# Performance work log

Hardware: AMD Instinct MI355X
Metric: run time of the kernel (lower is better)

The kernel has to match this reference:

```python
import jax, jax.numpy as jnp
import numpy as np

# pywt db4 reconstruction low-pass (rec_lo) coefficients.
_H = np.array([
    0.23037781330885523, 0.7148465705525415, 0.6308807679295904,
    -0.02798376941698385, -0.18703481171888114, 0.030841381835986965,
    0.032883011666982945, -0.010597401784997278], dtype=np.float64)
# pywt dec_lo = _H[::-1]; conv (flipped) correlation kernel = dec_lo[::-1] = _H.
_FLO = _H
# dec_hi[k] = (-1)^(7-k) * _H[k]; correlation kernel = dec_hi[::-1] -> (-1)^k * _H[7-k].
_FHI = np.array([(-1.0) ** k * _H[7 - k] for k in range(8)])
_FILT = jnp.asarray(np.stack([_FLO, _FHI])[:, None, :], dtype=jnp.float32)  # [2,1,8]
_PAD = 7  # filter_len - 1
_LEVEL = 4


def _dwt_step(sig):
    """One pywt dwt level, mode='symmetric'. sig: [N, L] -> (cA, cD), each [N, (L+7)//2]."""
    # symmetric (half-sample) extension by filter_len-1 each side, drop first sample
    # so that stride-2 VALID correlation reproduces pywt's output phase/length.
    xp = jnp.pad(sig, ((0, 0), (_PAD, _PAD)), mode='symmetric')[:, 1:]
    out = jax.lax.conv_general_dilated(
        xp[:, None, :], _FILT, window_strides=(2,), padding='VALID',
        dimension_numbers=('NCH', 'OIH', 'NCH'))  # [N, 2, (L+7)//2]
    return out[:, 0, :], out[:, 1, :]


def setup_inputs() -> dict:
    key = jax.random.key(0)
    x = jax.random.normal(key, (64, 4096, 32), dtype=jnp.float32)  # [B, L, C]
    return {"x": x}


def reference(x):
    """Faithful batched version of pywt.wavedec(x[i,:,j], 'db4', 'symmetric', level=4).
    Returns tuple (cA4, cD4, cD3, cD2, cD1), each [B, C, scale_len]."""
    B, L, C = x.shape
    sig = jnp.transpose(x, (0, 2, 1)).reshape(B * C, L)
    details = []
    for _ in range(_LEVEL):
        sig, cd = _dwt_step(sig)
        details.append(cd)
    coeffs = [sig] + details[::-1]  # [cA_L, cD_L, ..., cD_1] like pywt.wavedec
    return tuple(c.reshape(B, C, c.shape[-1]) for c in coeffs)
```

## Files before the change

### kernel.cpp

```cpp
#include <hip/hip_runtime.h>


#define NT 256
#define NCHB 2

#define LPX 634
#define LP1 322
#define LP2 166
#define LP3 86
#define CDPA 314
#define CDPB 154
#define CAP4 40

#define L0C 4096
#define L1C 2051
#define L2C 1029
#define L3C 518
#define L4C 262
#define SC 2048

#define OFF_CD4 (SC * L4C)
#define OFF_CD3 (2 * SC * L4C)
#define OFF_CD2 (OFF_CD3 + SC * L3C)
#define OFF_CD1 (OFF_CD2 + SC * L2C)

__device__ __forceinline__ void filt8(
    const float w0, const float w1, const float w2, const float w3,
    const float w4, const float w5, const float w6, const float w7,
    float& a, float& d) {
    constexpr float FLO[8] = {
        0.23037781330885523f,  0.7148465705525415f,  0.6308807679295904f,
        -0.02798376941698385f, -0.18703481171888114f, 0.030841381835986965f,
        0.032883011666982945f, -0.010597401784997278f};
    constexpr float FHI[8] = {
        -0.010597401784997278f, -0.032883011666982945f, 0.030841381835986965f,
        0.18703481171888114f,  -0.02798376941698385f,  -0.6308807679295904f,
        0.7148465705525415f,   -0.23037781330885523f};
    float a0 = FLO[0] * w0;
    a0 = fmaf(FLO[1], w1, a0); a0 = fmaf(FLO[2], w2, a0); a0 = fmaf(FLO[3], w3, a0);
    float a1 = FLO[4] * w4;
    a1 = fmaf(FLO[5], w5, a1); a1 = fmaf(FLO[6], w6, a1); a1 = fmaf(FLO[7], w7, a1);
    a = a0 + a1;
    float d0 = FHI[0] * w0;
    d0 = fmaf(FHI[1], w1, d0); d0 = fmaf(FHI[2], w2, d0); d0 = fmaf(FHI[3], w3, d0);
    float d1 = FHI[4] * w4;
    d1 = fmaf(FHI[5], w5, d1); d1 = fmaf(FHI[6], w6, d1); d1 = fmaf(FHI[7], w7, d1);
    d = d0 + d1;
}

template <int R, bool LAST>
__device__ __forceinline__ void level_run(
    const float* __restrict__ src, int PS, int srclo,
    float* __restrict__ dst, int PD, int DL,
    int lo, int hi,
    float* __restrict__ cdbuf, int CDP,
    float* __restrict__ cabuf,
    int c, int slot) {
    const int span = hi - lo;
    int i0r = slot * R;
    if (i0r > span - R) i0r = span - R;
    const int i0 = lo + i0r;

    const float2* row2 = reinterpret_cast<const float2*>(src + c * PS);
    int p = i0 - (srclo >> 1);
    float2 f0 = row2[p], f1 = row2[p + 1], f2 = row2[p + 2];
    float* drow = LAST ? nullptr : dst + c * PD;
    float* cdrow = cdbuf + c * CDP - lo;
    float* carow = LAST ? cabuf + c * CAP4 - lo : nullptr;

#pragma unroll
    for (int r = 0; r < R; ++r) {
        const float2 f3 = row2[p + 3 + r];
        const int i = i0 + r;
        float a, d;
        filt8(f0.x, f0.y, f1.x, f1.y, f2.x, f2.y, f3.x, f3.y, a, d);

        if constexpr (!LAST) {
            drow[i - lo + 6] = a;
            if (lo == 0 && i < 6) drow[5 - i] = a;
            if (hi == DL && i >= DL - 7) drow[(2 * DL - 1 - i) - lo + 6] = a;
        } else {
            carow[i] = a;
        }
        cdrow[i] = d;
        f0 = f1; f1 = f2; f2 = f3;
    }
}

__device__ __forceinline__ void dump_rows(
    const float* __restrict__ buf, int pitch, int bufLo,
    float* __restrict__ gbase, int rowLen, int ownLo, int ownHi, int tid) {
    const int span = ownHi - ownLo;
#pragma unroll
    for (int c2 = 0; c2 < NCHB; ++c2) {
        float* g = gbase + (size_t)c2 * rowLen + ownLo;
        const float* s = buf + c2 * pitch + (ownLo - bufLo);
        for (int i = tid; i < span; i += NT) g[i] = s[i];
    }
}

__global__ __launch_bounds__(NT, 8) void fused_dwt_kernel(
    const float* __restrict__ x, float* __restrict__ out) {
    __shared__ __align__(16) float bx[NCHB * LPX];
    __shared__ __align__(16) float b1[NCHB * LP1];
    __shared__ __align__(16) float b2[NCHB * LP2];
    __shared__ __align__(16) float b3[NCHB * LP3];
    __shared__ __align__(16) float cdA[NCHB * CDPA];
    __shared__ __align__(16) float cdB[NCHB * CDPB];
    __shared__ __align__(16) float caB[NCHB * CAP4];

    const int bid = blockIdx.x;
    const int work = (bid & 7) * 1024 + (bid >> 3);
    const int cg = work & 15;
    const int tile = (work >> 4) & 7;
    const int b = work >> 7;

    const int tid = threadIdx.x;
    const int c = tid & 1;
    const int slot = tid >> 1;
    const int c0 = cg * 2;
    const int sigB = b * 32 + c0;

    const int lo4 = 33 * tile, hi4 = min(L4C, lo4 + 33);
    const int lo3 = max(0, 2 * lo4 - 6), hi3 = min(L3C, 2 * hi4);
    const int lo2 = max(0, 2 * lo3 - 6), hi2 = min(L2C, 2 * hi3);
    const int lo1 = max(0, 2 * lo2 - 6), hi1 = min(L1C, 2 * hi2);
    const int lox = max(0, 2 * lo1 - 6), hix = min(L0C, 2 * hi1);

    const float* xb = x + (size_t)b * (L0C * 32) + c0;
    const int npair = (hix - lox) >> 1;
    for (int q = tid; q < npair; q += NT) {
        const int j = q << 1;
        const int t = lox + j;
        const float2 va = *reinterpret_cast<const float2*>(xb + (size_t)t * 32);
        const float2 vb = *reinterpret_cast<const float2*>(xb + (size_t)(t + 1) * 32);
        const float avv[2] = {va.x, va.y};
        const float bvv[2] = {vb.x, vb.y};
#pragma unroll
        for (int hh = 0; hh < NCHB; ++hh)
            *reinterpret_cast<float2*>(bx + hh * LPX + 6 + j) = make_float2(avv[hh], bvv[hh]);
        if (lox == 0 && t < 6) {
#pragma unroll
            for (int hh = 0; hh < NCHB; ++hh) {
                bx[hh * LPX + 5 - t] = avv[hh];
                if (t + 1 < 6) bx[hh * LPX + 4 - t] = bvv[hh];
            }
        }
        if (hix == L0C && t + 1 >= L0C - 7) {
#pragma unroll
            for (int hh = 0; hh < NCHB; ++hh) {
                if (t >= L0C - 7) bx[hh * LPX + (2 * L0C - 1 - t) - lox + 6] = avv[hh];
                bx[hh * LPX + (2 * L0C - 2 - t) - lox + 6] = bvv[hh];
            }
        }
    }
    __syncthreads();

    float* gca4 = out + (size_t)sigB * L4C;
    float* gcd4 = out + OFF_CD4 + (size_t)sigB * L4C;
    float* gcd3 = out + OFF_CD3 + (size_t)sigB * L3C;
    float* gcd2 = out + OFF_CD2 + (size_t)sigB * L2C;
    float* gcd1 = out + OFF_CD1 + (size_t)sigB * L1C;

    const int o1lo = tile ? 264 * tile - 34 : 0;
    const int o1hi = (tile == 7) ? L1C : 264 * tile + 230;
    const int o2lo = tile ? 132 * tile - 10 : 0;
    const int o2hi = (tile == 7) ? L2C : 132 * tile + 122;
    const int o3lo = tile ? 66 * tile - 2 : 0;
    const int o3hi = (tile == 7) ? L3C : 66 * tile + 64;

    level_run<3, false>(bx, LPX, lox, b1, LP1, L1C, lo1, hi1, cdA, CDPA, nullptr, c, slot);
    __syncthreads();

    dump_rows(cdA, CDPA, lo1, gcd1, L1C, o1lo, o1hi, tid);
    level_run<2, false>(b1, LP1, lo1, b2, LP2, L2C, lo2, hi2, cdB, CDPB, nullptr, c, slot);
    __syncthreads();

    dump_rows(cdB, CDPB, lo2, gcd2, L2C, o2lo, o2hi, tid);
    level_run<1, false>(b2, LP2, lo2, b3, LP3, L3C, lo3, hi3, cdA, CDPA, nullptr, c, slot);
    __syncthreads();

    dump_rows(cdA, CDPA, lo3, gcd3, L3C, o3lo, o3hi, tid);
    level_run<1, true>(b3, LP3, lo3, nullptr, 0, L4C, lo4, hi4, cdB, CDPB, caB, c, slot);
    __syncthreads();

    dump_rows(cdB, CDPB, lo4, gcd4, L4C, lo4, hi4, tid);
    dump_rows(caB, CAP4, lo4, gca4, L4C, lo4, hi4, tid);
}

extern "C" void kernel_launch(void* const* d_in, const int* in_sizes, int n_in,
                              void* d_out, int out_size, void* d_ws, size_t ws_size,
                              hipStream_t stream) {
    (void)in_sizes; (void)n_in; (void)d_ws; (void)ws_size; (void)out_size;
    const float* x = (const float*)d_in[0];
    float* out = (float*)d_out;
    fused_dwt_kernel<<<dim3(8192), dim3(NT), 0, stream>>>(x, out);
}
```

Baseline: 32.88 us.

## Process all 32 channels per block, read input directly from global, write outputs directly

Each block now handles one batch and one tile across all 32 channels, with 512 threads (32 channels x 16 slots), in place of 2 channels per block over 8192 blocks. Level 1 reads x straight from global memory with a sliding register window, and symmetric boundary handling is done through index mirroring only in edge tiles. Detail coefficients are written straight to global memory instead of being staged in shared memory and dumped afterwards. This removes the input staging pass and the extra copies, but global writes become strided per thread (each thread writes its own row), the grid shrinks to 512 blocks, and thread-to-work mapping and odd-span tail handling grow more complex.

```diff
diff --git a/kernel.cpp b/kernel.cpp
--- a/kernel.cpp
+++ b/kernel.cpp
@@ -1,16 +1,11 @@
 #include <hip/hip_runtime.h>
 
 
-#define NT 256
-#define NCHB 2
-
-#define LPX 634
+#define NT 512
+
 #define LP1 322
 #define LP2 166
 #define LP3 86
-#define CDPA 314
-#define CDPB 154
-#define CAP4 40
 
 #define L0C 4096
 #define L1C 2051
@@ -19,10 +14,16 @@
 #define L4C 262
 #define SC 2048
 
-#define OFF_CD4 (SC * L4C)
-#define OFF_CD3 (2 * SC * L4C)
-#define OFF_CD2 (OFF_CD3 + SC * L3C)
-#define OFF_CD1 (OFF_CD2 + SC * L2C)
+#define OFF_CD4 ((size_t)SC * L4C)
+#define OFF_CD3 ((size_t)2 * SC * L4C)
+#define OFF_CD2 (OFF_CD3 + (size_t)SC * L3C)
+#define OFF_CD1 (OFF_CD2 + (size_t)SC * L2C)
+
+__device__ __forceinline__ int sym_idx(int t, int L) {
+    if (t < 0) t = -1 - t;
+    if (t >= L) t = 2 * L - 1 - t;
+    return t;
+}
 
 __device__ __forceinline__ void filt8(
     const float w0, const float w1, const float w2, const float w3,
@@ -48,144 +49,173 @@
     d = d0 + d1;
 }
 
-template <int R, bool LAST>
-__device__ __forceinline__ void level_run(
-    const float* __restrict__ src, int PS, int srclo,
-    float* __restrict__ dst, int PD, int DL,
-    int lo, int hi,
-    float* __restrict__ cdbuf, int CDP,
-    float* __restrict__ cabuf,
-    int c, int slot) {
+template <bool MG>
+__device__ __forceinline__ void level1(
+    const float* __restrict__ xc,
+    float* __restrict__ b1row,
+    float* __restrict__ gcd1,
+    int lo1, int hi1, int slot) {
+    constexpr int R = 20;
+    const int span = hi1 - lo1;
+    const int i0 = lo1 + min(slot * R, (span - R) & ~1);
+    float w[8];
+#pragma unroll
+    for (int k = 0; k < 8; ++k) {
+        int t = 2 * i0 - 6 + k;
+        if (MG) t = sym_idx(t, L0C);
+        w[k] = xc[(size_t)t * 32];
+    }
+    float aprev = 0.f;
+#pragma unroll
+    for (int r = 0; r < R; ++r) {
+        const int i = i0 + r;
+        if (r) {
+#pragma unroll
+            for (int k = 0; k < 6; ++k) w[k] = w[k + 2];
+            int t0 = 2 * i, t1 = 2 * i + 1;
+            if (MG) { t0 = sym_idx(t0, L0C); t1 = sym_idx(t1, L0C); }
+            w[6] = xc[(size_t)t0 * 32];
+            w[7] = xc[(size_t)t1 * 32];
+        }
+        float a, d;
+        filt8(w[0], w[1], w[2], w[3], w[4], w[5], w[6], w[7], a, d);
+        gcd1[i] = d;
+        if (r & 1)
+            *reinterpret_cast<float2*>(b1row + (i - 1 - lo1 + 6)) = make_float2(aprev, a);
+        else
+            aprev = a;
+        if (MG) {
+            if (lo1 == 0 && i < 6) b1row[5 - i] = a;
+            if (hi1 == L1C && i >= L1C - 7) b1row[(2 * L1C - 1 - i) - lo1 + 6] = a;
+        }
+    }
+    if (MG && (span & 1) && slot == 15) {
+        const int i = hi1 - 1;
+        float ww[8];
+#pragma unroll
+        for (int k = 0; k < 8; ++k) ww[k] = xc[(size_t)sym_idx(2 * i - 6 + k, L0C) * 32];
+        float a, d;
+        filt8(ww[0], ww[1], ww[2], ww[3], ww[4], ww[5], ww[6], ww[7], a, d);
+        gcd1[i] = d;
+        b1row[i - lo1 + 6] = a;
+        if (hi1 == L1C && i >= L1C - 7) b1row[(2 * L1C - 1 - i) - lo1 + 6] = a;
+    }
+}
+
+template <int R, bool MG>
+__device__ __forceinline__ void levelmid(
+    const float* __restrict__ srow, int slo,
+    float* __restrict__ drow, int DL,
+    float* __restrict__ gcd,
+    int lo, int hi, int slot) {
     const int span = hi - lo;
-    int i0r = slot * R;
-    if (i0r > span - R) i0r = span - R;
-    const int i0 = lo + i0r;
-
-    const float2* row2 = reinterpret_cast<const float2*>(src + c * PS);
-    int p = i0 - (srclo >> 1);
-    float2 f0 = row2[p], f1 = row2[p + 1], f2 = row2[p + 2];
-    float* drow = LAST ? nullptr : dst + c * PD;
-    float* cdrow = cdbuf + c * CDP - lo;
-    float* carow = LAST ? cabuf + c * CAP4 - lo : nullptr;
-
+    const int i0 = lo + min(slot * R, (span - R) & ~1);
+    const float2* s2 = reinterpret_cast<const float2*>(srow);
+    const int p = i0 - (slo >> 1);
+    float2 f0 = s2[p], f1 = s2[p + 1], f2 = s2[p + 2];
+    float aprev = 0.f;
 #pragma unroll
     for (int r = 0; r < R; ++r) {
-        const float2 f3 = row2[p + 3 + r];
+        const float2 f3 = s2[p + 3 + r];
         const int i = i0 + r;
         float a, d;
         filt8(f0.x, f0.y, f1.x, f1.y, f2.x, f2.y, f3.x, f3.y, a, d);
-
-        if constexpr (!LAST) {
-            drow[i - lo + 6] = a;
+        gcd[i] = d;
+        if (r & 1)
+            *reinterpret_cast<float2*>(drow + (i - 1 - lo + 6)) = make_float2(aprev, a);
+        else
+            aprev = a;
+        if (MG) {
             if (lo == 0 && i < 6) drow[5 - i] = a;
             if (hi == DL && i >= DL - 7) drow[(2 * DL - 1 - i) - lo + 6] = a;
-        } else {
-            carow[i] = a;
-        }
-        cdrow[i] = d;
+        }
         f0 = f1; f1 = f2; f2 = f3;
     }
-}
-
-__device__ __forceinline__ void dump_rows(
-    const float* __restrict__ buf, int pitch, int bufLo,
-    float* __restrict__ gbase, int rowLen, int ownLo, int ownHi, int tid) {
-    const int span = ownHi - ownLo;
-#pragma unroll
-    for (int c2 = 0; c2 < NCHB; ++c2) {
-        float* g = gbase + (size_t)c2 * rowLen + ownLo;
-        const float* s = buf + c2 * pitch + (ownLo - bufLo);
-        for (int i = tid; i < span; i += NT) g[i] = s[i];
-    }
-}
-
-__global__ __launch_bounds__(NT, 8) void fused_dwt_kernel(
+    if (MG && (span & 1) && slot == 15) {
+        const int i = hi - 1;
+        const float* s = srow - slo + 6;
+        float a, d;
+        filt8(s[2*i-6], s[2*i-5], s[2*i-4], s[2*i-3], s[2*i-2], s[2*i-1], s[2*i], s[2*i+1], a, d);
+        gcd[i] = d;
+        drow[i - lo + 6] = a;
+        if (hi == DL && i >= DL - 7) drow[(2 * DL - 1 - i) - lo + 6] = a;
+    }
+}
+
+__device__ __forceinline__ void level4(
+    const float* __restrict__ srow, int slo,
+    float* __restrict__ gca, float* __restrict__ gcd,
+    int lo, int hi, int slot) {
+    const int span = hi - lo;
+    const int i0 = lo + min(slot * 3, span - 3);
+    const float* s = srow - slo + 6;
+    float w[8];
+#pragma unroll
+    for (int k = 0; k < 8; ++k) w[k] = s[2 * i0 - 6 + k];
+#pragma unroll
+    for (int r = 0; r < 3; ++r) {
+        const int i = i0 + r;
+        if (r) {
+#pragma unroll
+            for (int k = 0; k < 6; ++k) w[k] = w[k + 2];
+            w[6] = s[2 * i];
+            w[7] = s[2 * i + 1];
+        }
+        float a, d;
+        filt8(w[0], w[1], w[2], w[3], w[4], w[5], w[6], w[7], a, d);
+        gca[i] = a;
+        gcd[i] = d;
+    }
+}
+
+template <bool MG>
+__device__ __forceinline__ void cascade(
+    const float* xc, float* b1, float* b2, float* b3,
+    float* gcd1, float* gcd2, float* gcd3, float* gcd4, float* gca4,
+    int c, int slot,
+    int lo1, int hi1, int lo2, int hi2, int lo3, int hi3, int lo4, int hi4) {
+    level1<MG>(xc, b1 + c * LP1, gcd1, lo1, hi1, slot);
+    __syncthreads();
+    levelmid<10, MG>(b1 + c * LP1, lo1, b2 + c * LP2, L2C, gcd2, lo2, hi2, slot);
+    __syncthreads();
+    levelmid<6, MG>(b2 + c * LP2, lo2, b3 + c * LP3, L3C, gcd3, lo3, hi3, slot);
+    __syncthreads();
+    level4(b3 + c * LP3, lo3, gca4, gcd4, lo4, hi4, slot);
+}
+
+__global__ __launch_bounds__(NT, 4) void fused_dwt_kernel(
     const float* __restrict__ x, float* __restrict__ out) {
-    __shared__ __align__(16) float bx[NCHB * LPX];
-    __shared__ __align__(16) float b1[NCHB * LP1];
-    __shared__ __align__(16) float b2[NCHB * LP2];
-    __shared__ __align__(16) float b3[NCHB * LP3];
-    __shared__ __align__(16) float cdA[NCHB * CDPA];
-    __shared__ __align__(16) float cdB[NCHB * CDPB];
-    __shared__ __align__(16) float caB[NCHB * CAP4];
+    __shared__ __align__(16) float b1[32 * LP1];
+    __shared__ __align__(16) float b2[32 * LP2];
+    __shared__ __align__(16) float b3[32 * LP3];
 
     const int bid = blockIdx.x;
-    const int work = (bid & 7) * 1024 + (bid >> 3);
-    const int cg = work & 15;
-    const int tile = (work >> 4) & 7;
-    const int b = work >> 7;
+    const int tile = bid & 7;
+    const int b = bid >> 3;
 
     const int tid = threadIdx.x;
-    const int c = tid & 1;
-    const int slot = tid >> 1;
-    const int c0 = cg * 2;
-    const int sigB = b * 32 + c0;
+    const int c = tid & 31;
+    const int slot = tid >> 5;
 
     const int lo4 = 33 * tile, hi4 = min(L4C, lo4 + 33);
     const int lo3 = max(0, 2 * lo4 - 6), hi3 = min(L3C, 2 * hi4);
     const int lo2 = max(0, 2 * lo3 - 6), hi2 = min(L2C, 2 * hi3);
     const int lo1 = max(0, 2 * lo2 - 6), hi1 = min(L1C, 2 * hi2);
-    const int lox = max(0, 2 * lo1 - 6), hix = min(L0C, 2 * hi1);
-
-    const float* xb = x + (size_t)b * (L0C * 32) + c0;
-    const int npair = (hix - lox) >> 1;
-    for (int q = tid; q < npair; q += NT) {
-        const int j = q << 1;
-        const int t = lox + j;
-        const float2 va = *reinterpret_cast<const float2*>(xb + (size_t)t * 32);
-        const float2 vb = *reinterpret_cast<const float2*>(xb + (size_t)(t + 1) * 32);
-        const float avv[2] = {va.x, va.y};
-        const float bvv[2] = {vb.x, vb.y};
-#pragma unroll
-        for (int hh = 0; hh < NCHB; ++hh)
-            *reinterpret_cast<float2*>(bx + hh * LPX + 6 + j) = make_float2(avv[hh], bvv[hh]);
-        if (lox == 0 && t < 6) {
-#pragma unroll
-            for (int hh = 0; hh < NCHB; ++hh) {
-                bx[hh * LPX + 5 - t] = avv[hh];
-                if (t + 1 < 6) bx[hh * LPX + 4 - t] = bvv[hh];
-            }
-        }
-        if (hix == L0C && t + 1 >= L0C - 7) {
-#pragma unroll
-            for (int hh = 0; hh < NCHB; ++hh) {
-                if (t >= L0C - 7) bx[hh * LPX + (2 * L0C - 1 - t) - lox + 6] = avv[hh];
-                bx[hh * LPX + (2 * L0C - 2 - t) - lox + 6] = bvv[hh];
-            }
-        }
-    }
-    __syncthreads();
-
-    float* gca4 = out + (size_t)sigB * L4C;
-    float* gcd4 = out + OFF_CD4 + (size_t)sigB * L4C;
-    float* gcd3 = out + OFF_CD3 + (size_t)sigB * L3C;
-    float* gcd2 = out + OFF_CD2 + (size_t)sigB * L2C;
-    float* gcd1 = out + OFF_CD1 + (size_t)sigB * L1C;
-
-    const int o1lo = tile ? 264 * tile - 34 : 0;
-    const int o1hi = (tile == 7) ? L1C : 264 * tile + 230;
-    const int o2lo = tile ? 132 * tile - 10 : 0;
-    const int o2hi = (tile == 7) ? L2C : 132 * tile + 122;
-    const int o3lo = tile ? 66 * tile - 2 : 0;
-    const int o3hi = (tile == 7) ? L3C : 66 * tile + 64;
-
-    level_run<3, false>(bx, LPX, lox, b1, LP1, L1C, lo1, hi1, cdA, CDPA, nullptr, c, slot);
-    __syncthreads();
-
-    dump_rows(cdA, CDPA, lo1, gcd1, L1C, o1lo, o1hi, tid);
-    level_run<2, false>(b1, LP1, lo1, b2, LP2, L2C, lo2, hi2, cdB, CDPB, nullptr, c, slot);
-    __syncthreads();
-
-    dump_rows(cdB, CDPB, lo2, gcd2, L2C, o2lo, o2hi, tid);
-    level_run<1, false>(b2, LP2, lo2, b3, LP3, L3C, lo3, hi3, cdA, CDPA, nullptr, c, slot);
-    __syncthreads();
-
-    dump_rows(cdA, CDPA, lo3, gcd3, L3C, o3lo, o3hi, tid);
-    level_run<1, true>(b3, LP3, lo3, nullptr, 0, L4C, lo4, hi4, cdB, CDPB, caB, c, slot);
-    __syncthreads();
-
-    dump_rows(cdB, CDPB, lo4, gcd4, L4C, lo4, hi4, tid);
-    dump_rows(caB, CAP4, lo4, gca4, L4C, lo4, hi4, tid);
+
+    const int sig = b * 32 + c;
+    const float* xc = x + (size_t)b * (L0C * 32) + c;
+    float* gca4 = out + (size_t)sig * L4C;
+    float* gcd4 = out + OFF_CD4 + (size_t)sig * L4C;
+    float* gcd3 = out + OFF_CD3 + (size_t)sig * L3C;
+    float* gcd2 = out + OFF_CD2 + (size_t)sig * L2C;
+    float* gcd1 = out + OFF_CD1 + (size_t)sig * L1C;
+
+    if (tile == 0 || tile == 7)
+        cascade<true>(xc, b1, b2, b3, gcd1, gcd2, gcd3, gcd4, gca4, c, slot,
+                      lo1, hi1, lo2, hi2, lo3, hi3, lo4, hi4);
+    else
+        cascade<false>(xc, b1, b2, b3, gcd1, gcd2, gcd3, gcd4, gca4, c, slot,
+                       lo1, hi1, lo2, hi2, lo3, hi3, lo4, hi4);
 }
 
 extern "C" void kernel_launch(void* const* d_in, const int* in_sizes, int n_in,
@@ -194,5 +224,5 @@
     (void)in_sizes; (void)n_in; (void)d_ws; (void)ws_size; (void)out_size;
     const float* x = (const float*)d_in[0];
     float* out = (float*)d_out;
-    fused_dwt_kernel<<<dim3(8192), dim3(NT), 0, stream>>>(x, out);
-}
+    fused_dwt_kernel<<<dim3(512), dim3(NT), 0, stream>>>(x, out);
+}
```

New measurement: 49.68 us. 1.51x slower.
